# Kernel tuning notes

Measured on AMD Instinct MI355X. Metric: run time of the kernel, lower is better.

The kernel has to match this reference:

```python
import jax, jax.numpy as jnp
import numpy as np

K = 10  # hardcoded in the module
F = 3 + 3 * K + 3 * K + K + 3  # 76-dim per-point feature


def setup_inputs() -> dict:
    key = jax.random.key(0)
    k0, k1, k2, k3, k4 = jax.random.split(key, 5)
    B, N = 4, 8192
    input_cloud = jax.random.normal(k0, (B, N, 3), dtype=jnp.float32)
    # Single shared MLP (76 -> 64 -> 3); the original instantiates a fresh
    # randomly-initialized MLP per point, which a fused kernel replaces with
    # shared weights.
    W1 = jax.random.normal(k1, (F, 64), dtype=jnp.float32) * 0.1
    b1 = jax.random.normal(k2, (64,), dtype=jnp.float32) * 0.01
    W2 = jax.random.normal(k3, (64, 3), dtype=jnp.float32) * 0.1
    b2 = jax.random.normal(k4, (3,), dtype=jnp.float32) * 0.01
    return {"input_cloud": input_cloud, "W1": W1, "b1": b1, "W2": W2, "b2": b2}


def _knn_indices(cloud):
    # squared pairwise distances (same ordering as cdist), topk smallest
    sq = jnp.sum(cloud * cloud, axis=-1)  # [B,N]
    d2 = sq[:, :, None] + sq[:, None, :] - 2.0 * jnp.einsum("bnd,bmd->bnm", cloud, cloud)
    _, idx = jax.lax.top_k(-d2, K + 1)  # [B,N,K+1], smallest first (self at 0)
    return idx[:, :, 1:]  # drop self -> [B,N,K]


def reference(input_cloud, W1, b1, W2, b2):
    B, N, _ = input_cloud.shape
    knn_idx = _knn_indices(input_cloud)  # [B,N,K] int32

    # gather neighbors: [B,N,K,3]
    neighbors = jnp.take_along_axis(input_cloud[:, None, :, :],
                                    knn_idx[:, :, :, None], axis=2)
    center = input_cloud  # [B,N,3]
    rel = neighbors - center[:, :, None, :]           # [B,N,K,3]
    dists = jnp.sqrt(jnp.sum(rel * rel, axis=-1))     # [B,N,K]

    # per-point 3x3 covariance of the K neighbors (unbiased, like torch.cov)
    mean = jnp.mean(neighbors, axis=2, keepdims=True)  # [B,N,1,3]
    cen = neighbors - mean
    cov = jnp.einsum("bnki,bnkj->bnij", cen, cen) / (K - 1)  # [B,N,3,3]

    eig = jnp.linalg.eigvalsh(cov)          # ascending [B,N,3]
    l1, l2, l3 = eig[..., 2], eig[..., 1], eig[..., 0]  # descending order
    linearity = (l1 - l2) / l1
    planarity = (l2 - l3) / l1
    scattering = l3 / l1
    geom = jnp.stack([linearity, planarity, scattering], axis=-1)  # [B,N,3]

    feats = jnp.concatenate(
        [center,
         neighbors.reshape(B, N, 3 * K),
         rel.reshape(B, N, 3 * K),
         dists,
         geom], axis=-1)  # [B,N,76]

    h = jax.nn.relu(jnp.einsum("bnf,fh->bnh", feats, W1) + b1)
    out = jax.nn.relu(jnp.einsum("bnh,ho->bno", h, W2) + b2)  # [B,N,3]
    return out
```

## Files before the change

kernel.cpp:

```cpp
#include <hip/hip_runtime.h>
#include <math.h>

#define KNN    10
#define NPTS   8192
#define HID    64
#define NF     76
#define Q      16
#define CAP    64
#define F32_INF __uint_as_float(0x7F800000u)

__device__ __forceinline__ float rl(float v, int lane) {
    return __int_as_float(__builtin_amdgcn_readlane(__float_as_int(v), lane));
}

__global__ __launch_bounds__(256) void prep_kernel(const float* __restrict__ cloud,
                                                   float4* __restrict__ pts4) {
    const int i = blockIdx.x * 256 + threadIdx.x;
    const float x = cloud[i * 3 + 0];
    const float y = cloud[i * 3 + 1];
    const float z = cloud[i * 3 + 2];
    pts4[i] = make_float4(x, y, z, fmaf(z, z, fmaf(y, y, x * x)));
}

__global__ __launch_bounds__(1024) void knn_kernel(const float4* __restrict__ pts4,
                                                   unsigned short* __restrict__ knn_idx) {
    __shared__ unsigned long long coll[CAP][65];
    __shared__ float pk[16][Q][17];
    __shared__ float tau_s[64];
    __shared__ int   cnt[64];

    const int t    = threadIdx.x;
    const int w    = t >> 6;
    const int lane = t & 63;
    const int g    = w >> 2;
    const int h    = w & 3;
    const int bx   = blockIdx.x;
    const int b    = bx >> 7;
    const int n_base = (bx & 127) * 64 + g * Q;
    const int lq_base = g * Q;
    const int cb0 = h * (NPTS / 4);

    const float4* pb = pts4 + b * NPTS;

    if (t < 64) cnt[t] = 0;

    float qxs[Q], qys[Q], qzs[Q], qss[Q];
#pragma unroll
    for (int qq = 0; qq < Q; ++qq) {
        const float4 qv = pb[n_base + qq];
        qxs[qq] = qv.x; qys[qq] = qv.y; qzs[qq] = qv.z; qss[qq] = qv.w;
    }

    float vmin[Q];
#pragma unroll
    for (int qq = 0; qq < Q; ++qq) vmin[qq] = F32_INF;

    float4 cp = pb[cb0 + lane];
    for (int ti = 0; ti < NPTS / 4 / 64; ++ti) {
        const float4 np = (ti < NPTS / 4 / 64 - 1) ? pb[cb0 + (ti + 1) * 64 + lane] : cp;
        const float a2x = -2.0f * cp.x;
        const float a2y = -2.0f * cp.y;
        const float a2z = -2.0f * cp.z;
        const float aw  = cp.w;
#pragma unroll
        for (int qq = 0; qq < Q; ++qq) {
            const float v = fmaf(a2x, qxs[qq], fmaf(a2y, qys[qq], fmaf(a2z, qzs[qq], aw)));
            vmin[qq] = fminf(vmin[qq], v);
        }
        cp = np;
    }

#pragma unroll
    for (int qq = 0; qq < Q; ++qq) {
        float v = vmin[qq];
        v = fminf(v, __shfl_xor(v, 32, 64));
        v = fminf(v, __shfl_xor(v, 16, 64));
        if (lane < 16) pk[w][qq][lane] = v;
    }
    __syncthreads();

    if (h == 0) {
        float md[KNN + 1];
#pragma unroll
        for (int s = 0; s <= KNN; ++s) md[s] = F32_INF;
        const int qsel = lane & 15;
#pragma unroll
        for (int cc = 0; cc < 64; ++cc) {
            float d = pk[g * 4 + (cc >> 4)][qsel][cc & 15];
#pragma unroll
            for (int u = 0; u <= KNN; ++u) {
                const float lo = fminf(md[u], d);
                d = fmaxf(md[u], d);
                md[u] = lo;
            }
        }
        if (lane < 16) tau_s[lq_base + lane] = md[KNN] + 1e-3f;
    }
    __syncthreads();

    float taum[Q];
    {
        const float tv = tau_s[lq_base + (lane & 15)];
#pragma unroll
        for (int qq = 0; qq < Q; ++qq) taum[qq] = rl(tv, qq);
    }

    float4 cp2 = pb[cb0 + lane];
    int jcur = cb0 + lane;
    for (int ti = 0; ti < NPTS / 4 / 64; ++ti) {
        const float4 np = (ti < NPTS / 4 / 64 - 1) ? pb[cb0 + (ti + 1) * 64 + lane] : cp2;
        const float a2x = -2.0f * cp2.x;
        const float a2y = -2.0f * cp2.y;
        const float a2z = -2.0f * cp2.z;
        const float aw  = cp2.w;
#pragma unroll
        for (int qq = 0; qq < Q; ++qq) {
            const float v = fmaf(a2x, qxs[qq], fmaf(a2y, qys[qq], fmaf(a2z, qzs[qq], aw)));
            if (__builtin_expect(v <= taum[qq], 0)) {
                const float px = -0.5f * a2x;
                const float py = -0.5f * a2y;
                const float pz = -0.5f * a2z;
                const float dot = fmaf(pz, qzs[qq], fmaf(py, qys[qq], px * qxs[qq]));
                const float d2 = fmaf(-2.0f, dot, qss[qq] + aw);
                const unsigned int fb = __float_as_uint(d2);
                const unsigned int m =
                    fb ^ ((unsigned int)((int)fb >> 31) | 0x80000000u);
                const unsigned long long key =
                    ((unsigned long long)m << 13) | (unsigned long long)(unsigned)jcur;
                const int slot = atomicAdd(&cnt[lq_base + qq], 1);
                if (slot < CAP) coll[slot][lq_base + qq] = key;
            }
        }
        cp2 = np; jcur += 64;
    }
    __syncthreads();

    if (t < 64) {
        const int m = cnt[t];
        int mc = m;
#pragma unroll
        for (int off = 1; off < 64; off <<= 1)
            mc = max(mc, __shfl_xor(mc, off, 64));
        mc = __builtin_amdgcn_readfirstlane(mc);

        const int n = (bx & 127) * 64 + t;

        unsigned long long md[KNN + 1];
#pragma unroll
        for (int s = 0; s <= KNN; ++s) md[s] = ~0ULL;

        if (mc <= CAP) {
            for (int cc = 0; cc < mc; ++cc) {
                unsigned long long key = (cc < m) ? coll[cc][t] : ~0ULL;
#pragma unroll
                for (int u = 0; u <= KNN; ++u) {
                    const bool lt = key < md[u];
                    const unsigned long long lo = lt ? key : md[u];
                    key = lt ? md[u] : key;
                    md[u] = lo;
                }
            }
        } else {
            const float4 qv = pb[n];
            for (int j = 0; j < NPTS; ++j) {
                const float4 p = pb[j];
                const float dot = fmaf(p.z, qv.z, fmaf(p.y, qv.y, p.x * qv.x));
                const float d2 = fmaf(-2.0f, dot, qv.w + p.w);
                const unsigned int fb = __float_as_uint(d2);
                const unsigned int mm =
                    fb ^ ((unsigned int)((int)fb >> 31) | 0x80000000u);
                unsigned long long key =
                    ((unsigned long long)mm << 13) | (unsigned long long)j;
                key = (j == n) ? ~0ULL : key;
#pragma unroll
                for (int u = 0; u <= KNN; ++u) {
                    const bool lt = key < md[u];
                    const unsigned long long lo = lt ? key : md[u];
                    key = lt ? md[u] : key;
                    md[u] = lo;
                }
            }
        }

        unsigned short* outp = knn_idx + ((size_t)b * NPTS + n) * KNN;
        int outc = 0;
#pragma unroll
        for (int u = 0; u <= KNN; ++u) {
            const int idx = (int)(md[u] & 8191u);
            if (outc < KNN && idx != n) outp[outc++] = (unsigned short)idx;
        }
    }
}

__global__ __launch_bounds__(256) void feat_mlp_kernel(const float4* __restrict__ pts4,
                                                       const float* __restrict__ W1,
                                                       const float* __restrict__ b1,
                                                       const float* __restrict__ W2,
                                                       const float* __restrict__ b2,
                                                       const unsigned short* __restrict__ knn_idx,
                                                       float* __restrict__ out) {
    __shared__ float w1s[NF * 68];
    __shared__ float b1s[HID];
    __shared__ float w2s[HID * 3];
    __shared__ float b2s[3];
    __shared__ float fs[64][NF + 1];

    const int t = threadIdx.x;
    for (int idx = t; idx < NF * HID; idx += 256)
        w1s[(idx >> 6) * 68 + (idx & 63)] = W1[idx];
    if (t < HID) b1s[t] = b1[t];
    if (t < HID * 3) w2s[t] = W2[t];
    if (t < 3) b2s[t] = b2[t];

    const int pl   = t >> 2;
    const int subh = t & 1;
    const int subf = (t >> 1) & 1;
    const int gid = blockIdx.x * 64 + pl;
    const int b = gid >> 13;
    const int n = gid & (NPTS - 1);
    const float4* pb = pts4 + b * NPTS;

    if ((t & 3) == 0) {
        const float4 cq = pb[n];
        const float cx = cq.x, cy = cq.y, cz = cq.z;

        float nx[KNN], ny[KNN], nz[KNN];
        const unsigned short* ki = knn_idx + (size_t)gid * KNN;
#pragma unroll
        for (int k = 0; k < KNN; ++k) {
            const int j = ki[k];
            const float4 p = pb[j];
            nx[k] = p.x; ny[k] = p.y; nz[k] = p.z;
        }

        float* fr = fs[pl];
        fr[0] = cx; fr[1] = cy; fr[2] = cz;
#pragma unroll
        for (int k = 0; k < KNN; ++k) {
            fr[3 + 3 * k + 0] = nx[k];
            fr[3 + 3 * k + 1] = ny[k];
            fr[3 + 3 * k + 2] = nz[k];
        }
#pragma unroll
        for (int k = 0; k < KNN; ++k) {
            fr[33 + 3 * k + 0] = nx[k] - cx;
            fr[33 + 3 * k + 1] = ny[k] - cy;
            fr[33 + 3 * k + 2] = nz[k] - cz;
        }
#pragma unroll
        for (int k = 0; k < KNN; ++k) {
            const float rx = nx[k] - cx, ry = ny[k] - cy, rz = nz[k] - cz;
            fr[63 + k] = sqrtf(fmaf(rz, rz, fmaf(ry, ry, rx * rx)));
        }

        float mx = 0.f, my = 0.f, mz = 0.f;
#pragma unroll
        for (int k = 0; k < KNN; ++k) { mx += nx[k]; my += ny[k]; mz += nz[k]; }
        mx *= (1.0f / KNN); my *= (1.0f / KNN); mz *= (1.0f / KNN);
        float c00 = 0.f, c01 = 0.f, c02 = 0.f, c11 = 0.f, c12 = 0.f, c22 = 0.f;
#pragma unroll
        for (int k = 0; k < KNN; ++k) {
            const float ex = nx[k] - mx, ey = ny[k] - my, ez = nz[k] - mz;
            c00 = fmaf(ex, ex, c00); c01 = fmaf(ex, ey, c01); c02 = fmaf(ex, ez, c02);
            c11 = fmaf(ey, ey, c11); c12 = fmaf(ey, ez, c12); c22 = fmaf(ez, ez, c22);
        }
        const float sc = 1.0f / (KNN - 1);
        c00 *= sc; c01 *= sc; c02 *= sc; c11 *= sc; c12 *= sc; c22 *= sc;

        const float qd = (c00 + c11 + c22) * (1.0f / 3.0f);
        const float pp1 = c01 * c01 + c02 * c02 + c12 * c12;
        const float d00 = c00 - qd, d11 = c11 - qd, d22 = c22 - qd;
        const float p2 = d00 * d00 + d11 * d11 + d22 * d22 + 2.0f * pp1;
        float l1, l2, l3;
        if (p2 < 1e-30f) {
            l1 = l2 = l3 = qd;
        } else {
            const float p = sqrtf(p2 * (1.0f / 6.0f));
            const float inv = 1.0f / p;
            const float e00 = d00 * inv, e11 = d11 * inv, e22 = d22 * inv;
            const float e01 = c01 * inv, e02 = c02 * inv, e12 = c12 * inv;
            float detB = e00 * (e11 * e22 - e12 * e12)
                       - e01 * (e01 * e22 - e12 * e02)
                       + e02 * (e01 * e12 - e11 * e02);
            float r = 0.5f * detB;
            r = fminf(1.0f, fmaxf(-1.0f, r));
            const float phi = acosf(r) * (1.0f / 3.0f);
            l1 = qd + 2.0f * p * __cosf(phi);
            l3 = qd + 2.0f * p * __cosf(phi + 2.0943951023931953f);
            l2 = 3.0f * qd - l1 - l3;
        }
        fr[73] = (l1 - l2) / l1;
        fr[74] = (l2 - l3) / l1;
        fr[75] = l3 / l1;
    }

    __syncthreads();

    const float* fr = fs[pl];
    const int f0 = subf * 38;

    float h[32];
#pragma unroll
    for (int j = 0; j < 32; ++j) h[j] = (subf == 0) ? b1s[subh * 32 + j] : 0.0f;

#pragma unroll 2
    for (int ff = 0; ff < 38; ++ff) {
        const int f = f0 + ff;
        const float v = fr[f];
        const float4* w4 = reinterpret_cast<const float4*>(w1s + f * 68 + subh * 32);
#pragma unroll
        for (int j4 = 0; j4 < 8; ++j4) {
            const float4 w = w4[j4];
            h[4 * j4 + 0] = fmaf(v, w.x, h[4 * j4 + 0]);
            h[4 * j4 + 1] = fmaf(v, w.y, h[4 * j4 + 1]);
            h[4 * j4 + 2] = fmaf(v, w.z, h[4 * j4 + 2]);
            h[4 * j4 + 3] = fmaf(v, w.w, h[4 * j4 + 3]);
        }
    }

#pragma unroll
    for (int j = 0; j < 32; ++j) h[j] += __shfl_xor(h[j], 2, 64);

    float o0 = 0.f, o1 = 0.f, o2 = 0.f;
#pragma unroll
    for (int j = 0; j < 32; ++j) {
        const float r = fmaxf(h[j], 0.0f);
        const int jj = subh * 32 + j;
        o0 = fmaf(r, w2s[jj * 3 + 0], o0);
        o1 = fmaf(r, w2s[jj * 3 + 1], o1);
        o2 = fmaf(r, w2s[jj * 3 + 2], o2);
    }
    o0 += __shfl_xor(o0, 1, 64);
    o1 += __shfl_xor(o1, 1, 64);
    o2 += __shfl_xor(o2, 1, 64);

    if ((t & 3) == 0) {
        float* op = out + (size_t)gid * 3;
        op[0] = fmaxf(o0 + b2s[0], 0.0f);
        op[1] = fmaxf(o1 + b2s[1], 0.0f);
        op[2] = fmaxf(o2 + b2s[2], 0.0f);
    }
}

extern "C" void kernel_launch(void* const* d_in, const int* in_sizes, int n_in,
                              void* d_out, int out_size, void* d_ws, size_t ws_size,
                              hipStream_t stream) {
    const float* cloud = (const float*)d_in[0];
    const float* W1    = (const float*)d_in[1];
    const float* b1    = (const float*)d_in[2];
    const float* W2    = (const float*)d_in[3];
    const float* b2    = (const float*)d_in[4];
    float* out = (float*)d_out;

    float4* pts4 = (float4*)d_ws;
    unsigned short* knn = (unsigned short*)((char*)d_ws + 4 * NPTS * 16);

    prep_kernel<<<dim3(128), dim3(256), 0, stream>>>(cloud, pts4);
    knn_kernel<<<dim3(512), dim3(1024), 0, stream>>>(pts4, knn);
    feat_mlp_kernel<<<dim3(512), dim3(256), 0, stream>>>(pts4, W1, b1, W2, b2, knn, out);
}
```

Before: 183.2 us.

## Spread feature build and MLP across 16 lanes per point in feat kernel

The feature/MLP kernel now gives each point 16 threads instead of 4. Each of the first ten lanes gathers one neighbor and writes its features, and the mean and covariance come from shuffle reductions instead of one serial thread. The MLP work is split 4x4 over hidden units and features, with block size and grid doubled. This removes the single-thread-per-point feature bottleneck in the feat kernel, but every lane redundantly runs the eigen solve and there are more shuffles. The knn kernel, which likely dominates total time, is unchanged.

```diff
diff --git a/kernel.cpp b/kernel.cpp
--- a/kernel.cpp
+++ b/kernel.cpp
@@ -192,7 +192,7 @@
     }
 }
 
-__global__ __launch_bounds__(256) void feat_mlp_kernel(const float4* __restrict__ pts4,
+__global__ __launch_bounds__(512) void feat_mlp_kernel(const float4* __restrict__ pts4,
                                                        const float* __restrict__ W1,
                                                        const float* __restrict__ b1,
                                                        const float* __restrict__ W2,
@@ -203,70 +203,63 @@
     __shared__ float b1s[HID];
     __shared__ float w2s[HID * 3];
     __shared__ float b2s[3];
-    __shared__ float fs[64][NF + 1];
+    __shared__ float fs[32][NF + 2];
 
     const int t = threadIdx.x;
-    for (int idx = t; idx < NF * HID; idx += 256)
+    for (int idx = t; idx < NF * HID; idx += 512)
         w1s[(idx >> 6) * 68 + (idx & 63)] = W1[idx];
     if (t < HID) b1s[t] = b1[t];
     if (t < HID * 3) w2s[t] = W2[t];
     if (t < 3) b2s[t] = b2[t];
 
-    const int pl   = t >> 2;
-    const int subh = t & 1;
-    const int subf = (t >> 1) & 1;
-    const int gid = blockIdx.x * 64 + pl;
+    const int pl   = t >> 4;
+    const int s    = t & 15;
+    const int subh = s >> 2;
+    const int subf = s & 3;
+    const int gid = blockIdx.x * 32 + pl;
     const int b = gid >> 13;
     const int n = gid & (NPTS - 1);
     const float4* pb = pts4 + b * NPTS;
 
-    if ((t & 3) == 0) {
-        const float4 cq = pb[n];
-        const float cx = cq.x, cy = cq.y, cz = cq.z;
-
-        float nx[KNN], ny[KNN], nz[KNN];
-        const unsigned short* ki = knn_idx + (size_t)gid * KNN;
-#pragma unroll
-        for (int k = 0; k < KNN; ++k) {
-            const int j = ki[k];
-            const float4 p = pb[j];
-            nx[k] = p.x; ny[k] = p.y; nz[k] = p.z;
-        }
-
-        float* fr = fs[pl];
-        fr[0] = cx; fr[1] = cy; fr[2] = cz;
-#pragma unroll
-        for (int k = 0; k < KNN; ++k) {
-            fr[3 + 3 * k + 0] = nx[k];
-            fr[3 + 3 * k + 1] = ny[k];
-            fr[3 + 3 * k + 2] = nz[k];
-        }
-#pragma unroll
-        for (int k = 0; k < KNN; ++k) {
-            fr[33 + 3 * k + 0] = nx[k] - cx;
-            fr[33 + 3 * k + 1] = ny[k] - cy;
-            fr[33 + 3 * k + 2] = nz[k] - cz;
-        }
-#pragma unroll
-        for (int k = 0; k < KNN; ++k) {
-            const float rx = nx[k] - cx, ry = ny[k] - cy, rz = nz[k] - cz;
-            fr[63 + k] = sqrtf(fmaf(rz, rz, fmaf(ry, ry, rx * rx)));
-        }
-
-        float mx = 0.f, my = 0.f, mz = 0.f;
-#pragma unroll
-        for (int k = 0; k < KNN; ++k) { mx += nx[k]; my += ny[k]; mz += nz[k]; }
-        mx *= (1.0f / KNN); my *= (1.0f / KNN); mz *= (1.0f / KNN);
-        float c00 = 0.f, c01 = 0.f, c02 = 0.f, c11 = 0.f, c12 = 0.f, c22 = 0.f;
-#pragma unroll
-        for (int k = 0; k < KNN; ++k) {
-            const float ex = nx[k] - mx, ey = ny[k] - my, ez = nz[k] - mz;
-            c00 = fmaf(ex, ex, c00); c01 = fmaf(ex, ey, c01); c02 = fmaf(ex, ez, c02);
-            c11 = fmaf(ey, ey, c11); c12 = fmaf(ey, ez, c12); c22 = fmaf(ez, ez, c22);
-        }
-        const float sc = 1.0f / (KNN - 1);
-        c00 *= sc; c01 *= sc; c02 *= sc; c11 *= sc; c12 *= sc; c22 *= sc;
-
+    const float4 cq = pb[n];
+    const float cx = cq.x, cy = cq.y, cz = cq.z;
+
+    float nxv = 0.f, nyv = 0.f, nzv = 0.f;
+    if (s < KNN) {
+        const int j = knn_idx[(size_t)gid * KNN + s];
+        const float4 p = pb[j];
+        nxv = p.x; nyv = p.y; nzv = p.z;
+    }
+
+    float* fr = fs[pl];
+    if (s < KNN) {
+        fr[3 + 3 * s + 0] = nxv;
+        fr[3 + 3 * s + 1] = nyv;
+        fr[3 + 3 * s + 2] = nzv;
+        const float rx = nxv - cx, ry = nyv - cy, rz = nzv - cz;
+        fr[33 + 3 * s + 0] = rx;
+        fr[33 + 3 * s + 1] = ry;
+        fr[33 + 3 * s + 2] = rz;
+        fr[63 + s] = sqrtf(fmaf(rz, rz, fmaf(ry, ry, rx * rx)));
+    }
+    if (s == 10) { fr[0] = cx; fr[1] = cy; fr[2] = cz; }
+
+#define GSUM(v) { v += __shfl_xor(v, 1, 64); v += __shfl_xor(v, 2, 64); \
+                  v += __shfl_xor(v, 4, 64); v += __shfl_xor(v, 8, 64); }
+    float smx = nxv, smy = nyv, smz = nzv;
+    GSUM(smx); GSUM(smy); GSUM(smz);
+    const float mx = smx * 0.1f, my = smy * 0.1f, mz = smz * 0.1f;
+    const float ex = (s < KNN) ? nxv - mx : 0.f;
+    const float ey = (s < KNN) ? nyv - my : 0.f;
+    const float ez = (s < KNN) ? nzv - mz : 0.f;
+    float c00 = ex * ex, c01 = ex * ey, c02 = ex * ez;
+    float c11 = ey * ey, c12 = ey * ez, c22 = ez * ez;
+    GSUM(c00); GSUM(c01); GSUM(c02); GSUM(c11); GSUM(c12); GSUM(c22);
+#undef GSUM
+    const float sc = 1.0f / (KNN - 1);
+    c00 *= sc; c01 *= sc; c02 *= sc; c11 *= sc; c12 *= sc; c22 *= sc;
+
+    {
         const float qd = (c00 + c11 + c22) * (1.0f / 3.0f);
         const float pp1 = c01 * c01 + c02 * c02 + c12 * c12;
         const float d00 = c00 - qd, d11 = c11 - qd, d22 = c22 - qd;
@@ -289,52 +282,58 @@
             l3 = qd + 2.0f * p * __cosf(phi + 2.0943951023931953f);
             l2 = 3.0f * qd - l1 - l3;
         }
-        fr[73] = (l1 - l2) / l1;
-        fr[74] = (l2 - l3) / l1;
-        fr[75] = l3 / l1;
+        if (s == 0) {
+            fr[73] = (l1 - l2) / l1;
+            fr[74] = (l2 - l3) / l1;
+            fr[75] = l3 / l1;
+        }
     }
 
     __syncthreads();
 
-    const float* fr = fs[pl];
-    const int f0 = subf * 38;
-
-    float h[32];
-#pragma unroll
-    for (int j = 0; j < 32; ++j) h[j] = (subf == 0) ? b1s[subh * 32 + j] : 0.0f;
-
-#pragma unroll 2
-    for (int ff = 0; ff < 38; ++ff) {
-        const int f = f0 + ff;
-        const float v = fr[f];
-        const float4* w4 = reinterpret_cast<const float4*>(w1s + f * 68 + subh * 32);
-#pragma unroll
-        for (int j4 = 0; j4 < 8; ++j4) {
-            const float4 w = w4[j4];
-            h[4 * j4 + 0] = fmaf(v, w.x, h[4 * j4 + 0]);
-            h[4 * j4 + 1] = fmaf(v, w.y, h[4 * j4 + 1]);
-            h[4 * j4 + 2] = fmaf(v, w.z, h[4 * j4 + 2]);
-            h[4 * j4 + 3] = fmaf(v, w.w, h[4 * j4 + 3]);
-        }
-    }
-
-#pragma unroll
-    for (int j = 0; j < 32; ++j) h[j] += __shfl_xor(h[j], 2, 64);
+    const int f0 = subf * 19;
+    float h[16];
+#pragma unroll
+    for (int j = 0; j < 16; ++j) h[j] = (subf == 0) ? b1s[subh * 16 + j] : 0.0f;
+
+#pragma unroll
+    for (int ff = 0; ff < 19; ++ff) {
+        const float v = fr[f0 + ff];
+        const float4* w4 = reinterpret_cast<const float4*>(w1s + (f0 + ff) * 68 + subh * 16);
+#pragma unroll
+        for (int j4 = 0; j4 < 4; ++j4) {
+            const float4 wv = w4[j4];
+            h[4 * j4 + 0] = fmaf(v, wv.x, h[4 * j4 + 0]);
+            h[4 * j4 + 1] = fmaf(v, wv.y, h[4 * j4 + 1]);
+            h[4 * j4 + 2] = fmaf(v, wv.z, h[4 * j4 + 2]);
+            h[4 * j4 + 3] = fmaf(v, wv.w, h[4 * j4 + 3]);
+        }
+    }
+
+#pragma unroll
+    for (int j = 0; j < 16; ++j) {
+        h[j] += __shfl_xor(h[j], 1, 64);
+        h[j] += __shfl_xor(h[j], 2, 64);
+    }
 
     float o0 = 0.f, o1 = 0.f, o2 = 0.f;
 #pragma unroll
-    for (int j = 0; j < 32; ++j) {
+    for (int jj = 0; jj < 4; ++jj) {
+        const int j = subf * 4 + jj;
         const float r = fmaxf(h[j], 0.0f);
-        const int jj = subh * 32 + j;
-        o0 = fmaf(r, w2s[jj * 3 + 0], o0);
-        o1 = fmaf(r, w2s[jj * 3 + 1], o1);
-        o2 = fmaf(r, w2s[jj * 3 + 2], o2);
-    }
-    o0 += __shfl_xor(o0, 1, 64);
-    o1 += __shfl_xor(o1, 1, 64);
-    o2 += __shfl_xor(o2, 1, 64);
-
-    if ((t & 3) == 0) {
+        const int hidx = subh * 16 + j;
+        o0 = fmaf(r, w2s[hidx * 3 + 0], o0);
+        o1 = fmaf(r, w2s[hidx * 3 + 1], o1);
+        o2 = fmaf(r, w2s[hidx * 3 + 2], o2);
+    }
+#pragma unroll
+    for (int off = 1; off < 16; off <<= 1) {
+        o0 += __shfl_xor(o0, off, 64);
+        o1 += __shfl_xor(o1, off, 64);
+        o2 += __shfl_xor(o2, off, 64);
+    }
+
+    if (s == 0) {
         float* op = out + (size_t)gid * 3;
         op[0] = fmaxf(o0 + b2s[0], 0.0f);
         op[1] = fmaxf(o1 + b2s[1], 0.0f);
@@ -357,5 +356,5 @@
 
     prep_kernel<<<dim3(128), dim3(256), 0, stream>>>(cloud, pts4);
     knn_kernel<<<dim3(512), dim3(1024), 0, stream>>>(pts4, knn);
-    feat_mlp_kernel<<<dim3(512), dim3(256), 0, stream>>>(pts4, W1, b1, W2, b2, knn, out);
-}
+    feat_mlp_kernel<<<dim3(1024), dim3(512), 0, stream>>>(pts4, W1, b1, W2, b2, knn, out);
+}
```

New measurement: 189.5 us. 3.4% more time.
